# Performance work log

Hardware: AMD Instinct MI355X
Metric: run time of the kernel (lower is better)

The kernel has to match this reference:

```python
import jax, jax.numpy as jnp
import numpy as np

B, S, C = 4096, 512, 8
P, D, H, DFF, NL = 16, 64, 4, 96, 3
HID, HOR = 128, 24
TAU_MIN, TAU_MAX, NSTEPS = 0.05, 5.0, 32


def setup_inputs() -> dict:
    key = jax.random.key(0)
    ks = iter(jax.random.split(key, 40))
    n = lambda shape, s=0.05: (s * jax.random.normal(next(ks), shape)).astype(jnp.float32)
    return {
        "x": jax.random.normal(next(ks), (B, S, C), dtype=jnp.float32),
        "conv_w": n((D, C, P)),
        "conv_b": n((D,)),
        "cls": jax.random.normal(next(ks), (1, 1, D), dtype=jnp.float32),
        "attn_w": n((NL, 3 * D, D)),
        "attn_b": n((NL, 3 * D)),
        "out_w": n((NL, D, D)),
        "out_b": n((NL, D)),
        "ln1_g": jnp.ones((NL, D), jnp.float32),
        "ln1_b": jnp.zeros((NL, D), jnp.float32),
        "ln2_g": jnp.ones((NL, D), jnp.float32),
        "ln2_b": jnp.zeros((NL, D), jnp.float32),
        "ff1_w": n((NL, DFF, D)),
        "ff1_b": n((NL, DFF)),
        "ff2_w": n((NL, D, DFF)),
        "ff2_b": n((NL, D)),
        "B_mat": (0.02 * jax.random.normal(next(ks), (D, D))).astype(jnp.float32),
        "dr1_w": n((HID, D)),
        "dr1_b": n((HID,)),
        "dr2_w": n((D, HID)),
        "dr2_b": n((D,)),
        "tau1_w": n((HID, D + 1)),
        "tau1_b": n((HID,)),
        "tau2_w": n((D, HID)),
        "tau2_b": n((D,)),
        "fc_w": n((HOR * C, D)),
        "fc_b": n((HOR * C,)),
    }


def _layernorm(h, g, b, eps=1e-5):
    m = h.mean(-1, keepdims=True)
    v = ((h - m) ** 2).mean(-1, keepdims=True)
    return (h - m) / jnp.sqrt(v + eps) * g + b


def _pos_enc(L, d, dtype):
    pos = jnp.arange(L, dtype=dtype)[:, None]
    div = jnp.exp(jnp.arange(0, d, 2, dtype=dtype) * (-np.log(10000.0) / d))
    pe = jnp.zeros((L, d), dtype)
    pe = pe.at[:, 0::2].set(jnp.sin(pos * div))
    pe = pe.at[:, 1::2].set(jnp.cos(pos * div))
    return pe


def reference(x, conv_w, conv_b, cls, attn_w, attn_b, out_w, out_b,
              ln1_g, ln1_b, ln2_g, ln2_b, ff1_w, ff1_b, ff2_w, ff2_b,
              B_mat, dr1_w, dr1_b, dr2_w, dr2_b, tau1_w, tau1_b, tau2_w, tau2_b,
              fc_w, fc_b):
    bsz, s, c = x.shape
    n_p = s // P
    # PatchEmbed1D: Conv1d(kernel=stride=P) == per-patch linear projection
    xp = x.reshape(bsz, n_p, P, c)                       # [B,N,P,C]
    z = jnp.einsum('bnpc,dcp->bnd', xp, conv_w) + conv_b  # [B,N,D]
    z = jnp.concatenate([jnp.broadcast_to(cls, (bsz, 1, D)), z], axis=1)  # [B,N+1,D]
    L = z.shape[1]
    z = z + _pos_enc(L, D, z.dtype)
    hd = D // H
    scale = 1.0 / np.sqrt(hd)
    for l in range(NL):
        qkv = z @ attn_w[l].T + attn_b[l]                # [B,L,3D]
        q, k, v = jnp.split(qkv, 3, axis=-1)
        q = q.reshape(bsz, L, H, hd).transpose(0, 2, 1, 3)
        k = k.reshape(bsz, L, H, hd).transpose(0, 2, 1, 3)
        v = v.reshape(bsz, L, H, hd).transpose(0, 2, 1, 3)
        att = jax.nn.softmax(jnp.einsum('bhqd,bhkd->bhqk', q, k) * scale, axis=-1)
        o = jnp.einsum('bhqk,bhkd->bhqd', att, v).transpose(0, 2, 1, 3).reshape(bsz, L, D)
        o = o @ out_w[l].T + out_b[l]
        z = _layernorm(z + o, ln1_g[l], ln1_b[l])        # post-norm (torch default)
        f = jax.nn.relu(z @ ff1_w[l].T + ff1_b[l]) @ ff2_w[l].T + ff2_b[l]
        z = _layernorm(z + f, ln2_g[l], ln2_b[l])
    zc = z[:, 0]                                         # CLS token [B,D]
    # stable linear term A = -B^T B
    A = -(B_mat.T @ B_mat)
    h = 1.0 / NSTEPS

    def step(carry, _):
        zt, t = carry
        drive = jnp.tanh(zt @ dr1_w.T + dr1_b) @ dr2_w.T + dr2_b
        tt = jnp.full((zt.shape[0], 1), t, zt.dtype)
        tau_raw = jnp.tanh(jnp.concatenate([zt, tt], -1) @ tau1_w.T + tau1_b) @ tau2_w.T + tau2_b
        tau = TAU_MIN + (TAU_MAX - TAU_MIN) * jax.nn.sigmoid(jax.nn.softplus(tau_raw) + 1e-6)
        inv = 1.0 / tau
        dz = zt @ A.T + (-inv * zt + inv * drive)
        return (zt + h * dz, t + h), None

    (zt, _), _ = jax.lax.scan(step, (zc, jnp.float32(0.0)), None, length=NSTEPS)
    return zt @ fc_w.T + fc_b                            # [B, horizon*input_dim]
```

## Files before the change

### kernel.cpp

```cpp
#include <hip/hip_runtime.h>
#include <hip/hip_fp16.h>
#include <math.h>

#define DEV static __device__ __forceinline__

typedef _Float16 f16;
typedef __attribute__((ext_vector_type(4))) _Float16 f16x4;
typedef __attribute__((ext_vector_type(8))) _Float16 f16x8;
typedef __attribute__((ext_vector_type(4))) float f32x4;

DEV f16x8 ld8(const f16* p) { return *(const f16x8*)p; }
DEV f32x4 mfma32(f16x8 a, f16x8 b, f32x4 c) {
  return __builtin_amdgcn_mfma_f32_16x16x32_f16(a, b, c, 0, 0, 0);
}
DEV float ftanh(float x) {
  float e = __expf(2.f * x);
  return 1.f - 2.f / (e + 1.f);
}

__global__ __launch_bounds__(64) void prep_kernel(
    const float* __restrict__ Bm,
    const float* __restrict__ dr1_w, const float* __restrict__ dr1_b,
    const float* __restrict__ dr2_w, const float* __restrict__ dr2_b,
    const float* __restrict__ tau1_w, const float* __restrict__ tau1_b,
    const float* __restrict__ tau2_w, const float* __restrict__ tau2_b,
    const float* __restrict__ fc_w, const float* __restrict__ fc_b,
    char* __restrict__ wsb) {
  f16* dr1h = (f16*)(wsb);
  f16* tau1h = (f16*)(wsb + 16384);
  f16* dr2h = (f16*)(wsb + 32768);
  f16* tau2h = (f16*)(wsb + 49152);
  f16* Ah = (f16*)(wsb + 65536);
  f16* fch = (f16*)(wsb + 73728);
  float* fb = (float*)(wsb + 98304);

  const int t = threadIdx.x, blk = blockIdx.x;
  if (blk < 16) {
    int row = blk * 4 + (t >> 4), c0 = 4 * (t & 15);
    float a0 = 0.f, a1 = 0.f, a2 = 0.f, a3 = 0.f;
    for (int m = 0; m < 64; ++m) {
      float br = Bm[m * 64 + row];
      a0 = fmaf(br, Bm[m * 64 + c0 + 0], a0);
      a1 = fmaf(br, Bm[m * 64 + c0 + 1], a1);
      a2 = fmaf(br, Bm[m * 64 + c0 + 2], a2);
      a3 = fmaf(br, Bm[m * 64 + c0 + 3], a3);
    }
    Ah[row * 64 + c0 + 0] = (f16)(-a0);
    Ah[row * 64 + c0 + 1] = (f16)(-a1);
    Ah[row * 64 + c0 + 2] = (f16)(-a2);
    Ah[row * 64 + c0 + 3] = (f16)(-a3);
  } else if (blk < 48) {
    int idx = (blk - 16) * 64 + t;
    int row = idx >> 4, c0 = 4 * (idx & 15);
#pragma unroll
    for (int j = 0; j < 4; ++j) {
      dr1h[row * 64 + c0 + j] = (f16)dr1_w[row * 64 + c0 + j];
      tau1h[row * 64 + c0 + j] = (f16)tau1_w[row * 65 + c0 + j];
    }
  } else if (blk < 80) {
    int idx = (blk - 48) * 64 + t;
    int row = idx >> 5, c0 = 4 * (idx & 31);
#pragma unroll
    for (int j = 0; j < 4; ++j) {
      dr2h[row * 128 + c0 + j] = (f16)dr2_w[row * 128 + c0 + j];
      tau2h[row * 128 + c0 + j] = (f16)tau2_w[row * 128 + c0 + j];
    }
  } else if (blk < 128) {
    int idx = (blk - 80) * 64 + t;
    int row = idx >> 4, c0 = 4 * (idx & 15);
#pragma unroll
    for (int j = 0; j < 4; ++j)
      fch[row * 64 + c0 + j] = (f16)fc_w[row * 64 + c0 + j];
  } else {
    for (int i = (blk - 128) * 64 + t; i < 704; i += 128) {
      float v;
      if (i < 128) v = dr1_b[i];
      else if (i < 256) v = tau1_b[i - 128];
      else if (i < 320) v = dr2_b[i - 256];
      else if (i < 384) v = tau2_b[i - 320];
      else if (i < 512) v = tau1_w[(i - 384) * 65 + 64];
      else v = fc_b[i - 512];
      fb[i] = v;
    }
  }
}

__global__ __launch_bounds__(256) void prep_tf(
    const float* __restrict__ conv_w, const float* __restrict__ attn_w,
    const float* __restrict__ out_w, const float* __restrict__ ff1_w,
    const float* __restrict__ ff2_w, const float* __restrict__ conv_b,
    f16* __restrict__ tfw, float* __restrict__ pecb) {
  int idx = blockIdx.x * 256 + threadIdx.x;
  if (idx >= 96256) return;
  if (idx >= 94208) {
    int e = idx - 94208;
    int i = 1 + (e >> 6), dd = e & 63;
    float freq = __expf(-0.14391157f * (float)(dd & ~1));
    float ang = (float)i * freq;
    pecb[e] = ((dd & 1) ? cosf(ang) : sinf(ang)) + conv_b[dd];
    return;
  }
  float v;
  if (idx < 8192) {
    int dd = idx >> 7, k = idx & 127;
    v = conv_w[dd * 128 + (k & 7) * 16 + (k >> 3)];
  } else {
    int r = idx - 8192;
    int l = r / 28672, q = r - l * 28672;
    if (q < 12288) v = attn_w[l * 12288 + q];
    else if (q < 16384) v = out_w[l * 4096 + (q - 12288)];
    else if (q < 22528) v = ff1_w[l * 6144 + (q - 16384)];
    else v = ff2_w[l * 6144 + (q - 22528)];
  }
  tfw[idx] = (f16)v;
}

__global__ __launch_bounds__(256, 3) void tf_kernel(
    const float* __restrict__ x, const f16* __restrict__ tfw,
    const float* __restrict__ pecb, const float* __restrict__ cls,
    const float* __restrict__ attn_b, const float* __restrict__ out_b,
    const float* __restrict__ ln1_g, const float* __restrict__ ln1_b,
    const float* __restrict__ ln2_g, const float* __restrict__ ln2_b,
    const float* __restrict__ ff1_b, const float* __restrict__ ff2_b,
    float* __restrict__ zc) {
  __shared__ __align__(16) unsigned char SH[52240];
  float* Zm = (float*)SH;
  f16* Zh = (f16*)(SH + 8976);
  f16* Qh = (f16*)(SH + 15888);
  f16* Kh = (f16*)(SH + 22800);
  f16* VT = (f16*)(SH + 29712);
  f16* P = (f16*)(SH + 36880);
  f16* Sx = (f16*)(SH + 15888);
  f16* f1h = (f16*)(SH + 22800);
  f16* oh = Qh;

  const int t = threadIdx.x;
  const int b = blockIdx.x;
  const int w = t >> 6, lane = t & 63;
  const int c16 = lane & 15, q4 = lane >> 4;
  const int dcol = w * 16 + c16;
  const int d4 = w * 16 + q4 * 4;
  const int nrow = t >> 2, nl4 = t & 3;

  {
    const float4* xg = (const float4*)(x + (size_t)b * 4096);
    for (int i = t; i < 1024; i += 256) {
      int n = i >> 5, jj = i & 31;
      float4 v = xg[i];
      *(f16x4*)(Sx + n * 136 + jj * 4) = f16x4{(f16)v.x, (f16)v.y, (f16)v.z, (f16)v.w};
    }
    unsigned* zp = (unsigned*)(Zh + 33 * 72);
    for (int i = t; i < 540; i += 256) zp[i] = 0u;
    uint4 z4{0, 0, 0, 0};
    uint4* pp = (uint4*)P;
    for (int i = t; i < 960; i += 256) pp[i] = z4;
    if (t < 64) {
      float v = cls[t] + ((t & 1) ? 1.0f : 0.0f);
      Zm[t] = v; Zh[t] = (f16)v;
    }
  }
  __syncthreads();

  {
    f16x8 cw[4];
#pragma unroll
    for (int kb = 0; kb < 4; ++kb)
      cw[kb] = ld8(tfw + dcol * 128 + kb * 32 + q4 * 8);
#pragma unroll
    for (int it = 0; it < 2; ++it) {
      f32x4 acc = {};
#pragma unroll
      for (int kb = 0; kb < 4; ++kb)
        acc = mfma32(cw[kb], ld8(Sx + (it * 16 + c16) * 136 + kb * 32 + q4 * 8), acc);
      int n = it * 16 + c16;
      float4 pe = *(const float4*)(pecb + n * 64 + d4);
      float4 o{acc[0] + pe.x, acc[1] + pe.y, acc[2] + pe.z, acc[3] + pe.w};
      *(float4*)(Zm + (n + 1) * 68 + d4) = o;
      *(f16x4*)(Zh + (n + 1) * 72 + d4) = f16x4{(f16)o.x, (f16)o.y, (f16)o.z, (f16)o.w};
    }
  }
  __syncthreads();

  for (int l = 0; l < 3; ++l) {
    const f16* lw = tfw + 8192 + l * 28672;
    const int ntile = (l == 2) ? 1 : 3;
    const bool has2 = (w < 2);
    const int j1f = has2 ? (w + 4) * 16 + c16 : dcol;
    const int j1b = has2 ? (w + 4) * 16 + q4 * 4 : d4;

    f16x8 wq0 = ld8(lw + dcol * 64 + q4 * 8);
    f16x8 wq1 = ld8(lw + dcol * 64 + 32 + q4 * 8);
    f16x8 wk0 = ld8(lw + (64 + dcol) * 64 + q4 * 8);
    f16x8 wk1 = ld8(lw + (64 + dcol) * 64 + 32 + q4 * 8);
    f16x8 wv0 = ld8(lw + (128 + dcol) * 64 + q4 * 8);
    f16x8 wv1 = ld8(lw + (128 + dcol) * 64 + 32 + q4 * 8);
    f16x8 ow0 = ld8(lw + 12288 + dcol * 64 + q4 * 8);
    f16x8 ow1 = ld8(lw + 12288 + dcol * 64 + 32 + q4 * 8);
    f16x8 f1w00 = ld8(lw + 16384 + dcol * 64 + q4 * 8);
    f16x8 f1w01 = ld8(lw + 16384 + dcol * 64 + 32 + q4 * 8);
    f16x8 f1w10 = ld8(lw + 16384 + j1f * 64 + q4 * 8);
    f16x8 f1w11 = ld8(lw + 16384 + j1f * 64 + 32 + q4 * 8);
    f16x8 fw20 = ld8(lw + 22528 + dcol * 96 + q4 * 8);
    f16x8 fw21 = ld8(lw + 22528 + dcol * 96 + 32 + q4 * 8);
    f16x8 fw22 = ld8(lw + 22528 + dcol * 96 + 64 + q4 * 8);
    float4 bq4 = *(const float4*)(attn_b + l * 192 + d4);
    float4 bk4 = *(const float4*)(attn_b + l * 192 + 64 + d4);
    float bv = attn_b[l * 192 + 128 + dcol];
    float4 ob4 = *(const float4*)(out_b + l * 64 + d4);
    float4 f1b0 = *(const float4*)(ff1_b + l * 96 + d4);
    float4 f1b1 = *(const float4*)(ff1_b + l * 96 + j1b);
    float4 f2b4 = *(const float4*)(ff2_b + l * 64 + d4);

    {
      f16x8 zr0[3], zr1[3];
#pragma unroll
      for (int it = 0; it < 3; ++it) {
        zr0[it] = ld8(Zh + (it * 16 + c16) * 72 + q4 * 8);
        zr1[it] = ld8(Zh + (it * 16 + c16) * 72 + 32 + q4 * 8);
      }
#pragma unroll
      for (int it = 0; it < 3; ++it) {
        f32x4 aq = {}, ak = {}, av = {};
        aq = mfma32(wq0, zr0[it], aq); aq = mfma32(wq1, zr1[it], aq);
        ak = mfma32(wk0, zr0[it], ak); ak = mfma32(wk1, zr1[it], ak);
        av = mfma32(zr0[it], wv0, av); av = mfma32(zr1[it], wv1, av);
        int i = it * 16 + c16;
        *(f16x4*)(Qh + i * 72 + d4) =
            f16x4{(f16)((aq[0] + bq4.x) * 0.25f), (f16)((aq[1] + bq4.y) * 0.25f),
                  (f16)((aq[2] + bq4.z) * 0.25f), (f16)((aq[3] + bq4.w) * 0.25f)};
        *(f16x4*)(Kh + i * 72 + d4) =
            f16x4{(f16)(ak[0] + bk4.x), (f16)(ak[1] + bk4.y),
                  (f16)(ak[2] + bk4.z), (f16)(ak[3] + bk4.w)};
        if (it < 2) {
          *(f16x4*)(VT + dcol * 56 + it * 16 + q4 * 4) =
              f16x4{(f16)(av[0] + bv), (f16)(av[1] + bv),
                    (f16)(av[2] + bv), (f16)(av[3] + bv)};
        } else if (q4 == 0) {
          VT[dcol * 56 + 32] = (f16)(av[0] + bv);
        }
      }
    }

    {
      f16x8 zf = {};
      f16x8 kf0 = (q4 < 2) ? ld8(Kh + (c16) * 72 + w * 16 + q4 * 8) : zf;
      f16x8 kf1 = (q4 < 2) ? ld8(Kh + (16 + c16) * 72 + w * 16 + q4 * 8) : zf;
      f16x8 kf2 = (q4 < 2) ? ld8(Kh + (32 + c16) * 72 + w * 16 + q4 * 8) : zf;
      f16x8 vf = ld8(VT + dcol * 56 + q4 * 8);
      float vt32[4];
#pragma unroll
      for (int r = 0; r < 4; ++r) vt32[r] = (float)VT[(d4 + r) * 56 + 32];
      f16* Ph = P + w * 1920;
#pragma unroll
      for (int it = 0; it < 3; ++it) {
        if (it >= ntile) break;
        f16x8 qf = (q4 < 2) ? ld8(Qh + (it * 16 + c16) * 72 + w * 16 + q4 * 8) : zf;
        f32x4 zz = {};
        f32x4 s0 = mfma32(kf0, qf, zz);
        f32x4 s1 = mfma32(kf1, qf, zz);
        f32x4 s2 = mfma32(kf2, qf, zz);
        float m = -1e30f;
#pragma unroll
        for (int r = 0; r < 4; ++r) m = fmaxf(m, fmaxf(s0[r], s1[r]));
        if (q4 == 0) m = fmaxf(m, s2[0]);
        m = fmaxf(m, __shfl_xor(m, 16));
        m = fmaxf(m, __shfl_xor(m, 32));
        float e0[4], e1[4], su = 0.f;
#pragma unroll
        for (int r = 0; r < 4; ++r) {
          e0[r] = __expf(s0[r] - m); e1[r] = __expf(s1[r] - m);
          su += e0[r] + e1[r];
        }
        float e2 = (q4 == 0) ? __expf(s2[0] - m) : 0.f;
        su += e2;
        su += __shfl_xor(su, 16);
        su += __shfl_xor(su, 32);
        float inv = 1.f / su;
        int i = it * 16 + c16;
        *(f16x4*)(Ph + i * 40 + q4 * 4) =
            f16x4{(f16)(e0[0] * inv), (f16)(e0[1] * inv),
                  (f16)(e0[2] * inv), (f16)(e0[3] * inv)};
        *(f16x4*)(Ph + i * 40 + 16 + q4 * 4) =
            f16x4{(f16)(e1[0] * inv), (f16)(e1[1] * inv),
                  (f16)(e1[2] * inv), (f16)(e1[3] * inv)};
        if (q4 == 0) Ph[i * 40 + 32] = (f16)(e2 * inv);
      }
#pragma unroll
      for (int it = 0; it < 3; ++it) {
        if (it >= ntile) break;
        int i = it * 16 + c16;
        f16x8 pf = ld8(Ph + i * 40 + q4 * 8);
        f32x4 zz = {};
        f32x4 acc = mfma32(vf, pf, zz);
        float p32 = (float)Ph[i * 40 + 32];
        *(f16x4*)(oh + i * 72 + d4) =
            f16x4{(f16)(acc[0] + vt32[0] * p32), (f16)(acc[1] + vt32[1] * p32),
                  (f16)(acc[2] + vt32[2] * p32), (f16)(acc[3] + vt32[3] * p32)};
      }
    }
    __syncthreads();

#pragma unroll
    for (int it = 0; it < 3; ++it) {
      if (it >= ntile) break;
      int i = it * 16 + c16;
      f32x4 acc = {};
      acc = mfma32(ow0, ld8(oh + i * 72 + q4 * 8), acc);
      acc = mfma32(ow1, ld8(oh + i * 72 + 32 + q4 * 8), acc);
      if (it < 2 || c16 == 0) {
        float4 z = *(float4*)(Zm + i * 68 + d4);
        z.x += acc[0] + ob4.x; z.y += acc[1] + ob4.y;
        z.z += acc[2] + ob4.z; z.w += acc[3] + ob4.w;
        *(float4*)(Zm + i * 68 + d4) = z;
      }
    }
    __syncthreads();

    {
      int rows = (l == 2) ? 16 : 33;
      if (nrow < rows) {
        const float4* zr = (const float4*)(Zm + nrow * 68 + nl4 * 16);
        float4 zv[4];
        float su = 0.f, ss = 0.f;
#pragma unroll
        for (int g4 = 0; g4 < 4; ++g4) {
          float4 v = zr[g4];
          zv[g4] = v;
          su += (v.x + v.y) + (v.z + v.w);
          ss = fmaf(v.x, v.x, ss); ss = fmaf(v.y, v.y, ss);
          ss = fmaf(v.z, v.z, ss); ss = fmaf(v.w, v.w, ss);
        }
        su += __shfl_xor(su, 1); ss += __shfl_xor(ss, 1);
        su += __shfl_xor(su, 2); ss += __shfl_xor(ss, 2);
        float m = su * 0.015625f;
        float rr = rsqrtf(ss * 0.015625f - m * m + 1e-5f);
        const float4* gg = (const float4*)(ln1_g + l * 64 + nl4 * 16);
        const float4* bb = (const float4*)(ln1_b + l * 64 + nl4 * 16);
        float4* zw = (float4*)(Zm + nrow * 68 + nl4 * 16);
        f16* zh = Zh + nrow * 72 + nl4 * 16;
#pragma unroll
        for (int g4 = 0; g4 < 4; ++g4) {
          float4 G = gg[g4], B = bb[g4], v = zv[g4];
          float4 o;
          o.x = (v.x - m) * rr * G.x + B.x;
          o.y = (v.y - m) * rr * G.y + B.y;
          o.z = (v.z - m) * rr * G.z + B.z;
          o.w = (v.w - m) * rr * G.w + B.w;
          zw[g4] = o;
          *(f16x4*)(zh + g4 * 4) = f16x4{(f16)o.x, (f16)o.y, (f16)o.z, (f16)o.w};
        }
      }
    }
    __syncthreads();

    {
      f16x8 zr0[3], zr1[3];
#pragma unroll
      for (int it = 0; it < 3; ++it) {
        zr0[it] = ld8(Zh + (it * 16 + c16) * 72 + q4 * 8);
        zr1[it] = ld8(Zh + (it * 16 + c16) * 72 + 32 + q4 * 8);
      }
#pragma unroll
      for (int it = 0; it < 3; ++it) {
        if (it >= ntile) break;
        int i = it * 16 + c16;
        f32x4 acc = {};
        acc = mfma32(f1w00, zr0[it], acc);
        acc = mfma32(f1w01, zr1[it], acc);
        *(f16x4*)(f1h + i * 104 + d4) =
            f16x4{(f16)fmaxf(acc[0] + f1b0.x, 0.f), (f16)fmaxf(acc[1] + f1b0.y, 0.f),
                  (f16)fmaxf(acc[2] + f1b0.z, 0.f), (f16)fmaxf(acc[3] + f1b0.w, 0.f)};
        if (has2) {
          f32x4 a2 = {};
          a2 = mfma32(f1w10, zr0[it], a2);
          a2 = mfma32(f1w11, zr1[it], a2);
          *(f16x4*)(f1h + i * 104 + j1b) =
              f16x4{(f16)fmaxf(a2[0] + f1b1.x, 0.f), (f16)fmaxf(a2[1] + f1b1.y, 0.f),
                    (f16)fmaxf(a2[2] + f1b1.z, 0.f), (f16)fmaxf(a2[3] + f1b1.w, 0.f)};
        }
      }
    }
    __syncthreads();

#pragma unroll
    for (int it = 0; it < 3; ++it) {
      if (it >= ntile) break;
      int i = it * 16 + c16;
      f32x4 acc = {};
      acc = mfma32(fw20, ld8(f1h + i * 104 + q4 * 8), acc);
      acc = mfma32(fw21, ld8(f1h + i * 104 + 32 + q4 * 8), acc);
      acc = mfma32(fw22, ld8(f1h + i * 104 + 64 + q4 * 8), acc);
      if (it < 2 || c16 == 0) {
        float4 z = *(float4*)(Zm + i * 68 + d4);
        z.x += acc[0] + f2b4.x; z.y += acc[1] + f2b4.y;
        z.z += acc[2] + f2b4.z; z.w += acc[3] + f2b4.w;
        *(float4*)(Zm + i * 68 + d4) = z;
      }
    }
    __syncthreads();

    {
      int rows = (l == 2) ? 1 : 33;
      if (nrow < rows) {
        const float4* zr = (const float4*)(Zm + nrow * 68 + nl4 * 16);
        float4 zv[4];
        float su = 0.f, ss = 0.f;
#pragma unroll
        for (int g4 = 0; g4 < 4; ++g4) {
          float4 v = zr[g4];
          zv[g4] = v;
          su += (v.x + v.y) + (v.z + v.w);
          ss = fmaf(v.x, v.x, ss); ss = fmaf(v.y, v.y, ss);
          ss = fmaf(v.z, v.z, ss); ss = fmaf(v.w, v.w, ss);
        }
        su += __shfl_xor(su, 1); ss += __shfl_xor(ss, 1);
        su += __shfl_xor(su, 2); ss += __shfl_xor(ss, 2);
        float m = su * 0.015625f;
        float rr = rsqrtf(ss * 0.015625f - m * m + 1e-5f);
        const float4* gg = (const float4*)(ln2_g + l * 64 + nl4 * 16);
        const float4* bb = (const float4*)(ln2_b + l * 64 + nl4 * 16);
        if (l == 2) {
          float4* zo = (float4*)(zc + (size_t)b * 64 + nl4 * 16);
#pragma unroll
          for (int g4 = 0; g4 < 4; ++g4) {
            float4 G = gg[g4], B = bb[g4], v = zv[g4];
            float4 o;
            o.x = (v.x - m) * rr * G.x + B.x;
            o.y = (v.y - m) * rr * G.y + B.y;
            o.z = (v.z - m) * rr * G.z + B.z;
            o.w = (v.w - m) * rr * G.w + B.w;
            zo[g4] = o;
          }
        } else {
          float4* zw = (float4*)(Zm + nrow * 68 + nl4 * 16);
          f16* zh = Zh + nrow * 72 + nl4 * 16;
#pragma unroll
          for (int g4 = 0; g4 < 4; ++g4) {
            float4 G = gg[g4], B = bb[g4], v = zv[g4];
            float4 o;
            o.x = (v.x - m) * rr * G.x + B.x;
            o.y = (v.y - m) * rr * G.y + B.y;
            o.z = (v.z - m) * rr * G.z + B.z;
            o.w = (v.w - m) * rr * G.w + B.w;
            zw[g4] = o;
            *(f16x4*)(zh + g4 * 4) = f16x4{(f16)o.x, (f16)o.y, (f16)o.z, (f16)o.w};
          }
        }
      }
    }
    __syncthreads();
  }
}

__global__ __launch_bounds__(256, 1) void ode_kernel(
    const char* __restrict__ wsb, const float* __restrict__ zc,
    float* __restrict__ out) {
  const f16* dr1h = (const f16*)(wsb);
  const f16* tau1h = (const f16*)(wsb + 16384);
  const f16* Ah = (const f16*)(wsb + 65536);
  const f16* fch = (const f16*)(wsb + 73728);
  const float* fb = (const float*)(wsb + 98304);

  __shared__ __align__(16) f16 dr2s[64 * 128];
  __shared__ __align__(16) f16 tau2s[64 * 128];
  __shared__ __align__(16) f16 ztL[16 * 64];
  __shared__ __align__(16) f16 hdL[16 * 128];
  __shared__ __align__(16) f16 htL[16 * 128];

  const int t = threadIdx.x;
  const int w = t >> 6;
  const int lane = t & 63;
  const int c16 = lane & 15, q4 = lane >> 4;
  const int b0 = blockIdx.x * 16;
  const int swz = (c16 & 7) << 3;

  for (int i = t; i < 2048; i += 256) {
    int m = i >> 10, gi = i & 1023, row = gi >> 4, g = gi & 15;
    uint4 v = ((const uint4*)(wsb + 32768 + m * 16384))[gi];
    ((uint4*)(m ? tau2s : dr2s))[row * 16 + (g ^ (row & 7))] = v;
  }

  f16x8 dr1B[2][2], tau1B[2][2], AB[2];
#pragma unroll
  for (int j = 0; j < 2; ++j) {
    int cth = w * 2 + j;
#pragma unroll
    for (int kb = 0; kb < 2; ++kb) {
      dr1B[j][kb] = ld8(dr1h + (cth * 16 + c16) * 64 + kb * 32 + q4 * 8);
      tau1B[j][kb] = ld8(tau1h + (cth * 16 + c16) * 64 + kb * 32 + q4 * 8);
    }
  }
#pragma unroll
  for (int kb = 0; kb < 2; ++kb)
    AB[kb] = ld8(Ah + (w * 16 + c16) * 64 + kb * 32 + q4 * 8);
  float dr1b[2], tau1b[2], t1t[2];
#pragma unroll
  for (int j = 0; j < 2; ++j) {
    int cc = (w * 2 + j) * 16 + c16;
    dr1b[j] = fb[cc]; tau1b[j] = fb[128 + cc]; t1t[j] = fb[384 + cc];
  }
  float dr2b = fb[256 + w * 16 + c16];
  float tau2b = fb[320 + w * 16 + c16];

  float zt[4];
#pragma unroll
  for (int r = 0; r < 4; ++r)
    zt[r] = zc[(size_t)(b0 + q4 * 4 + r) * 64 + w * 16 + c16];

  __syncthreads();

  float tm = 0.f;
  for (int s = 0; s < 32; ++s) {
#pragma unroll
    for (int r = 0; r < 4; ++r) {
      int row = q4 * 4 + r;
      ztL[row * 64 + ((w * 16 + c16) ^ ((row & 7) << 3))] = (f16)zt[r];
    }
    __syncthreads();
    f16x8 ztA[2];
#pragma unroll
    for (int kb = 0; kb < 2; ++kb)
      ztA[kb] = ld8(ztL + c16 * 64 + ((kb * 32 + q4 * 8) ^ swz));

#pragma unroll
    for (int j = 0; j < 2; ++j) {
      f32x4 ad = {}, at = {};
      ad = mfma32(ztA[0], dr1B[j][0], ad);
      ad = mfma32(ztA[1], dr1B[j][1], ad);
      at = mfma32(ztA[0], tau1B[j][0], at);
      at = mfma32(ztA[1], tau1B[j][1], at);
      float bt = fmaf(tm, t1t[j], tau1b[j]);
      int colbase = (w * 2 + j) * 16 + c16;
#pragma unroll
      for (int r = 0; r < 4; ++r) {
        int row = q4 * 4 + r;
        int off = row * 128 + (colbase ^ ((row & 7) << 3));
        hdL[off] = (f16)ftanh(ad[r] + dr1b[j]);
        htL[off] = (f16)ftanh(at[r] + bt);
      }
    }
    __syncthreads();
    f16x8 hdA[4], htA[4];
#pragma unroll
    for (int kb = 0; kb < 4; ++kb) {
      int ko = c16 * 128 + ((kb * 32 + q4 * 8) ^ swz);
      hdA[kb] = ld8(hdL + ko);
      htA[kb] = ld8(htL + ko);
    }

    {
      int row16 = (w * 16 + c16) * 128;
      f32x4 dv = {}, tr = {}, za = {};
#pragma unroll
      for (int kb = 0; kb < 4; ++kb) {
        f16x8 bd = ld8(dr2s + row16 + ((kb * 32 + q4 * 8) ^ swz));
        f16x8 bt2 = ld8(tau2s + row16 + ((kb * 32 + q4 * 8) ^ swz));
        dv = mfma32(hdA[kb], bd, dv);
        tr = mfma32(htA[kb], bt2, tr);
      }
      za = mfma32(ztA[0], AB[0], za);
      za = mfma32(ztA[1], AB[1], za);
#pragma unroll
      for (int r = 0; r < 4; ++r) {
        float traw = tr[r] + tau2b;
        float sp = (traw > 15.f) ? traw : log1pf(__expf(traw));
        float sg = 1.f / (1.f + __expf(-(sp + 1e-6f)));
        float inv = 1.f / fmaf(4.95f, sg, 0.05f);
        float ztv = zt[r];
        float dz = za[r] + inv * ((dv[r] + dr2b) - ztv);
        zt[r] = fmaf(0.03125f, dz, ztv);
      }
    }
    tm += 0.03125f;
  }

#pragma unroll
  for (int r = 0; r < 4; ++r) {
    int row = q4 * 4 + r;
    ztL[row * 64 + ((w * 16 + c16) ^ ((row & 7) << 3))] = (f16)zt[r];
  }
  __syncthreads();
  f16x8 zA2[2];
#pragma unroll
  for (int kb = 0; kb < 2; ++kb)
    zA2[kb] = ld8(ztL + c16 * 64 + ((kb * 32 + q4 * 8) ^ swz));
#pragma unroll
  for (int j = 0; j < 3; ++j) {
    int ct = w * 3 + j;
    f32x4 acc = {};
    acc = mfma32(zA2[0], ld8(fch + (ct * 16 + c16) * 64 + q4 * 8), acc);
    acc = mfma32(zA2[1], ld8(fch + (ct * 16 + c16) * 64 + 32 + q4 * 8), acc);
    float bias = fb[512 + ct * 16 + c16];
#pragma unroll
    for (int r = 0; r < 4; ++r)
      out[(size_t)(b0 + q4 * 4 + r) * 192 + ct * 16 + c16] = acc[r] + bias;
  }
}

extern "C" void kernel_launch(void* const* d_in, const int* in_sizes, int n_in,
                              void* d_out, int out_size, void* d_ws, size_t ws_size,
                              hipStream_t stream) {
  const float* x = (const float*)d_in[0];
  const float* conv_w = (const float*)d_in[1];
  const float* conv_b = (const float*)d_in[2];
  const float* cls = (const float*)d_in[3];
  const float* attn_w = (const float*)d_in[4];
  const float* attn_b = (const float*)d_in[5];
  const float* out_w = (const float*)d_in[6];
  const float* out_b = (const float*)d_in[7];
  const float* ln1_g = (const float*)d_in[8];
  const float* ln1_b = (const float*)d_in[9];
  const float* ln2_g = (const float*)d_in[10];
  const float* ln2_b = (const float*)d_in[11];
  const float* ff1_w = (const float*)d_in[12];
  const float* ff1_b = (const float*)d_in[13];
  const float* ff2_w = (const float*)d_in[14];
  const float* ff2_b = (const float*)d_in[15];
  const float* B_mat = (const float*)d_in[16];
  const float* dr1_w = (const float*)d_in[17];
  const float* dr1_b = (const float*)d_in[18];
  const float* dr2_w = (const float*)d_in[19];
  const float* dr2_b = (const float*)d_in[20];
  const float* tau1_w = (const float*)d_in[21];
  const float* tau1_b = (const float*)d_in[22];
  const float* tau2_w = (const float*)d_in[23];
  const float* tau2_b = (const float*)d_in[24];
  const float* fc_w = (const float*)d_in[25];
  const float* fc_b = (const float*)d_in[26];

  char* wsb = (char*)d_ws;
  float* zcb = (float*)(wsb + 101376);
  f16* tfw = (f16*)(wsb + 1149952);
  float* pecb = (float*)(wsb + 1338368);

  prep_kernel<<<130, 64, 0, stream>>>(B_mat, dr1_w, dr1_b, dr2_w, dr2_b,
                                      tau1_w, tau1_b, tau2_w, tau2_b,
                                      fc_w, fc_b, wsb);
  prep_tf<<<376, 256, 0, stream>>>(conv_w, attn_w, out_w, ff1_w, ff2_w, conv_b,
                                   tfw, pecb);
  tf_kernel<<<4096, 256, 0, stream>>>(x, tfw, pecb, cls, attn_b, out_b,
                                      ln1_g, ln1_b, ln2_g, ln2_b, ff1_b, ff2_b, zcb);
  ode_kernel<<<256, 256, 0, stream>>>(wsb, zcb, (float*)d_out);
}
```

Baseline: 269.7 us.

## Drop fp32 residual buffer in transformer LDS and split ODE batch across more blocks

The transformer kernel drops its fp32 residual copy and keeps the residual stream only in fp16 shared memory. The VT and P buffers are compacted, which cuts LDS from about 52KB to 39KB so four blocks can fit per CU instead of three. The ODE kernel now handles 8 batch rows per block over 512 blocks, with the 16-row MFMA tile half duplicated, so more of the GPU is used on the serial 32-step loop. The cost is fp16 rounding on the residual accumulation, and half of the ODE MFMA work is redundant.

```diff
diff --git a/kernel.cpp b/kernel.cpp
--- a/kernel.cpp
+++ b/kernel.cpp
@@ -115,7 +115,7 @@
   tfw[idx] = (f16)v;
 }
 
-__global__ __launch_bounds__(256, 3) void tf_kernel(
+__global__ __launch_bounds__(256, 4) void tf_kernel(
     const float* __restrict__ x, const f16* __restrict__ tfw,
     const float* __restrict__ pecb, const float* __restrict__ cls,
     const float* __restrict__ attn_b, const float* __restrict__ out_b,
@@ -123,15 +123,14 @@
     const float* __restrict__ ln2_g, const float* __restrict__ ln2_b,
     const float* __restrict__ ff1_b, const float* __restrict__ ff2_b,
     float* __restrict__ zc) {
-  __shared__ __align__(16) unsigned char SH[52240];
-  float* Zm = (float*)SH;
-  f16* Zh = (f16*)(SH + 8976);
-  f16* Qh = (f16*)(SH + 15888);
-  f16* Kh = (f16*)(SH + 22800);
-  f16* VT = (f16*)(SH + 29712);
-  f16* P = (f16*)(SH + 36880);
-  f16* Sx = (f16*)(SH + 15888);
-  f16* f1h = (f16*)(SH + 22800);
+  __shared__ __align__(16) unsigned char SH[38800];
+  f16* Zh = (f16*)SH;
+  f16* Qh = (f16*)(SH + 6912);
+  f16* Kh = (f16*)(SH + 13824);
+  f16* VT = (f16*)(SH + 20736);
+  f16* P = (f16*)(SH + 25856);
+  f16* Sx = (f16*)(SH + 6912);
+  f16* f1h = (f16*)(SH + 13824);
   f16* oh = Qh;
 
   const int t = threadIdx.x;
@@ -153,11 +152,8 @@
     for (int i = t; i < 540; i += 256) zp[i] = 0u;
     uint4 z4{0, 0, 0, 0};
     uint4* pp = (uint4*)P;
-    for (int i = t; i < 960; i += 256) pp[i] = z4;
-    if (t < 64) {
-      float v = cls[t] + ((t & 1) ? 1.0f : 0.0f);
-      Zm[t] = v; Zh[t] = (f16)v;
-    }
+    for (int i = t; i < 809; i += 256) pp[i] = z4;
+    if (t < 64) Zh[t] = (f16)(cls[t] + ((t & 1) ? 1.0f : 0.0f));
   }
   __syncthreads();
 
@@ -174,9 +170,9 @@
         acc = mfma32(cw[kb], ld8(Sx + (it * 16 + c16) * 136 + kb * 32 + q4 * 8), acc);
       int n = it * 16 + c16;
       float4 pe = *(const float4*)(pecb + n * 64 + d4);
-      float4 o{acc[0] + pe.x, acc[1] + pe.y, acc[2] + pe.z, acc[3] + pe.w};
-      *(float4*)(Zm + (n + 1) * 68 + d4) = o;
-      *(f16x4*)(Zh + (n + 1) * 72 + d4) = f16x4{(f16)o.x, (f16)o.y, (f16)o.z, (f16)o.w};
+      *(f16x4*)(Zh + (n + 1) * 72 + d4) =
+          f16x4{(f16)(acc[0] + pe.x), (f16)(acc[1] + pe.y),
+                (f16)(acc[2] + pe.z), (f16)(acc[3] + pe.w)};
     }
   }
   __syncthreads();
@@ -232,11 +228,11 @@
             f16x4{(f16)(ak[0] + bk4.x), (f16)(ak[1] + bk4.y),
                   (f16)(ak[2] + bk4.z), (f16)(ak[3] + bk4.w)};
         if (it < 2) {
-          *(f16x4*)(VT + dcol * 56 + it * 16 + q4 * 4) =
+          *(f16x4*)(VT + dcol * 40 + it * 16 + q4 * 4) =
               f16x4{(f16)(av[0] + bv), (f16)(av[1] + bv),
                     (f16)(av[2] + bv), (f16)(av[3] + bv)};
         } else if (q4 == 0) {
-          VT[dcol * 56 + 32] = (f16)(av[0] + bv);
+          VT[dcol * 40 + 32] = (f16)(av[0] + bv);
         }
       }
     }
@@ -246,11 +242,11 @@
       f16x8 kf0 = (q4 < 2) ? ld8(Kh + (c16) * 72 + w * 16 + q4 * 8) : zf;
       f16x8 kf1 = (q4 < 2) ? ld8(Kh + (16 + c16) * 72 + w * 16 + q4 * 8) : zf;
       f16x8 kf2 = (q4 < 2) ? ld8(Kh + (32 + c16) * 72 + w * 16 + q4 * 8) : zf;
-      f16x8 vf = ld8(VT + dcol * 56 + q4 * 8);
+      f16x8 vf = ld8(VT + dcol * 40 + q4 * 8);
       float vt32[4];
 #pragma unroll
-      for (int r = 0; r < 4; ++r) vt32[r] = (float)VT[(d4 + r) * 56 + 32];
-      f16* Ph = P + w * 1920;
+      for (int r = 0; r < 4; ++r) vt32[r] = (float)VT[(d4 + r) * 40 + 32];
+      f16* Ph = P + w * 1320;
 #pragma unroll
       for (int it = 0; it < 3; ++it) {
         if (it >= ntile) break;
@@ -277,13 +273,15 @@
         su += __shfl_xor(su, 32);
         float inv = 1.f / su;
         int i = it * 16 + c16;
-        *(f16x4*)(Ph + i * 40 + q4 * 4) =
-            f16x4{(f16)(e0[0] * inv), (f16)(e0[1] * inv),
-                  (f16)(e0[2] * inv), (f16)(e0[3] * inv)};
-        *(f16x4*)(Ph + i * 40 + 16 + q4 * 4) =
-            f16x4{(f16)(e1[0] * inv), (f16)(e1[1] * inv),
-                  (f16)(e1[2] * inv), (f16)(e1[3] * inv)};
-        if (q4 == 0) Ph[i * 40 + 32] = (f16)(e2 * inv);
+        if (i < 33) {
+          *(f16x4*)(Ph + i * 40 + q4 * 4) =
+              f16x4{(f16)(e0[0] * inv), (f16)(e0[1] * inv),
+                    (f16)(e0[2] * inv), (f16)(e0[3] * inv)};
+          *(f16x4*)(Ph + i * 40 + 16 + q4 * 4) =
+              f16x4{(f16)(e1[0] * inv), (f16)(e1[1] * inv),
+                    (f16)(e1[2] * inv), (f16)(e1[3] * inv)};
+          if (q4 == 0) Ph[i * 40 + 32] = (f16)(e2 * inv);
+        }
       }
 #pragma unroll
       for (int it = 0; it < 3; ++it) {
@@ -308,10 +306,12 @@
       acc = mfma32(ow0, ld8(oh + i * 72 + q4 * 8), acc);
       acc = mfma32(ow1, ld8(oh + i * 72 + 32 + q4 * 8), acc);
       if (it < 2 || c16 == 0) {
-        float4 z = *(float4*)(Zm + i * 68 + d4);
-        z.x += acc[0] + ob4.x; z.y += acc[1] + ob4.y;
-        z.z += acc[2] + ob4.z; z.w += acc[3] + ob4.w;
-        *(float4*)(Zm + i * 68 + d4) = z;
+        f16x4 zr = *(f16x4*)(Zh + i * 72 + d4);
+        *(f16x4*)(Zh + i * 72 + d4) =
+            f16x4{(f16)((float)zr[0] + acc[0] + ob4.x),
+                  (f16)((float)zr[1] + acc[1] + ob4.y),
+                  (f16)((float)zr[2] + acc[2] + ob4.z),
+                  (f16)((float)zr[3] + acc[3] + ob4.w)};
       }
     }
     __syncthreads();
@@ -319,35 +319,28 @@
     {
       int rows = (l == 2) ? 16 : 33;
       if (nrow < rows) {
-        const float4* zr = (const float4*)(Zm + nrow * 68 + nl4 * 16);
-        float4 zv[4];
+        f16* zr = Zh + nrow * 72 + nl4 * 16;
+        f16x8 h0 = ld8(zr), h1 = ld8(zr + 8);
+        float v[16];
+#pragma unroll
+        for (int j = 0; j < 8; ++j) { v[j] = (float)h0[j]; v[8 + j] = (float)h1[j]; }
         float su = 0.f, ss = 0.f;
 #pragma unroll
-        for (int g4 = 0; g4 < 4; ++g4) {
-          float4 v = zr[g4];
-          zv[g4] = v;
-          su += (v.x + v.y) + (v.z + v.w);
-          ss = fmaf(v.x, v.x, ss); ss = fmaf(v.y, v.y, ss);
-          ss = fmaf(v.z, v.z, ss); ss = fmaf(v.w, v.w, ss);
-        }
+        for (int j = 0; j < 16; ++j) { su += v[j]; ss = fmaf(v[j], v[j], ss); }
         su += __shfl_xor(su, 1); ss += __shfl_xor(ss, 1);
         su += __shfl_xor(su, 2); ss += __shfl_xor(ss, 2);
         float m = su * 0.015625f;
         float rr = rsqrtf(ss * 0.015625f - m * m + 1e-5f);
         const float4* gg = (const float4*)(ln1_g + l * 64 + nl4 * 16);
         const float4* bb = (const float4*)(ln1_b + l * 64 + nl4 * 16);
-        float4* zw = (float4*)(Zm + nrow * 68 + nl4 * 16);
-        f16* zh = Zh + nrow * 72 + nl4 * 16;
 #pragma unroll
         for (int g4 = 0; g4 < 4; ++g4) {
-          float4 G = gg[g4], B = bb[g4], v = zv[g4];
-          float4 o;
-          o.x = (v.x - m) * rr * G.x + B.x;
-          o.y = (v.y - m) * rr * G.y + B.y;
-          o.z = (v.z - m) * rr * G.z + B.z;
-          o.w = (v.w - m) * rr * G.w + B.w;
-          zw[g4] = o;
-          *(f16x4*)(zh + g4 * 4) = f16x4{(f16)o.x, (f16)o.y, (f16)o.z, (f16)o.w};
+          float4 G = gg[g4], B = bb[g4];
+          *(f16x4*)(zr + g4 * 4) =
+              f16x4{(f16)((v[g4 * 4 + 0] - m) * rr * G.x + B.x),
+                    (f16)((v[g4 * 4 + 1] - m) * rr * G.y + B.y),
+                    (f16)((v[g4 * 4 + 2] - m) * rr * G.z + B.z),
+                    (f16)((v[g4 * 4 + 3] - m) * rr * G.w + B.w)};
         }
       }
     }
@@ -391,10 +384,12 @@
       acc = mfma32(fw21, ld8(f1h + i * 104 + 32 + q4 * 8), acc);
       acc = mfma32(fw22, ld8(f1h + i * 104 + 64 + q4 * 8), acc);
       if (it < 2 || c16 == 0) {
-        float4 z = *(float4*)(Zm + i * 68 + d4);
-        z.x += acc[0] + f2b4.x; z.y += acc[1] + f2b4.y;
-        z.z += acc[2] + f2b4.z; z.w += acc[3] + f2b4.w;
-        *(float4*)(Zm + i * 68 + d4) = z;
+        f16x4 zr = *(f16x4*)(Zh + i * 72 + d4);
+        *(f16x4*)(Zh + i * 72 + d4) =
+            f16x4{(f16)((float)zr[0] + acc[0] + f2b4.x),
+                  (f16)((float)zr[1] + acc[1] + f2b4.y),
+                  (f16)((float)zr[2] + acc[2] + f2b4.z),
+                  (f16)((float)zr[3] + acc[3] + f2b4.w)};
       }
     }
     __syncthreads();
@@ -402,17 +397,14 @@
     {
       int rows = (l == 2) ? 1 : 33;
       if (nrow < rows) {
-        const float4* zr = (const float4*)(Zm + nrow * 68 + nl4 * 16);
-        float4 zv[4];
+        f16* zr = Zh + nrow * 72 + nl4 * 16;
+        f16x8 h0 = ld8(zr), h1 = ld8(zr + 8);
+        float v[16];
+#pragma unroll
+        for (int j = 0; j < 8; ++j) { v[j] = (float)h0[j]; v[8 + j] = (float)h1[j]; }
         float su = 0.f, ss = 0.f;
 #pragma unroll
-        for (int g4 = 0; g4 < 4; ++g4) {
-          float4 v = zr[g4];
-          zv[g4] = v;
-          su += (v.x + v.y) + (v.z + v.w);
-          ss = fmaf(v.x, v.x, ss); ss = fmaf(v.y, v.y, ss);
-          ss = fmaf(v.z, v.z, ss); ss = fmaf(v.w, v.w, ss);
-        }
+        for (int j = 0; j < 16; ++j) { su += v[j]; ss = fmaf(v[j], v[j], ss); }
         su += __shfl_xor(su, 1); ss += __shfl_xor(ss, 1);
         su += __shfl_xor(su, 2); ss += __shfl_xor(ss, 2);
         float m = su * 0.015625f;
@@ -423,27 +415,21 @@
           float4* zo = (float4*)(zc + (size_t)b * 64 + nl4 * 16);
 #pragma unroll
           for (int g4 = 0; g4 < 4; ++g4) {
-            float4 G = gg[g4], B = bb[g4], v = zv[g4];
-            float4 o;
-            o.x = (v.x - m) * rr * G.x + B.x;
-            o.y = (v.y - m) * rr * G.y + B.y;
-            o.z = (v.z - m) * rr * G.z + B.z;
-            o.w = (v.w - m) * rr * G.w + B.w;
-            zo[g4] = o;
+            float4 G = gg[g4], B = bb[g4];
+            zo[g4] = make_float4((v[g4 * 4 + 0] - m) * rr * G.x + B.x,
+                                 (v[g4 * 4 + 1] - m) * rr * G.y + B.y,
+                                 (v[g4 * 4 + 2] - m) * rr * G.z + B.z,
+                                 (v[g4 * 4 + 3] - m) * rr * G.w + B.w);
           }
         } else {
-          float4* zw = (float4*)(Zm + nrow * 68 + nl4 * 16);
-          f16* zh = Zh + nrow * 72 + nl4 * 16;
 #pragma unroll
           for (int g4 = 0; g4 < 4; ++g4) {
-            float4 G = gg[g4], B = bb[g4], v = zv[g4];
-            float4 o;
-            o.x = (v.x - m) * rr * G.x + B.x;
-            o.y = (v.y - m) * rr * G.y + B.y;
-            o.z = (v.z - m) * rr * G.z + B.z;
-            o.w = (v.w - m) * rr * G.w + B.w;
-            zw[g4] = o;
-            *(f16x4*)(zh + g4 * 4) = f16x4{(f16)o.x, (f16)o.y, (f16)o.z, (f16)o.w};
+            float4 G = gg[g4], B = bb[g4];
+            *(f16x4*)(zr + g4 * 4) =
+                f16x4{(f16)((v[g4 * 4 + 0] - m) * rr * G.x + B.x),
+                      (f16)((v[g4 * 4 + 1] - m) * rr * G.y + B.y),
+                      (f16)((v[g4 * 4 + 2] - m) * rr * G.z + B.z),
+                      (f16)((v[g4 * 4 + 3] - m) * rr * G.w + B.w)};
           }
         }
       }
@@ -452,7 +438,7 @@
   }
 }
 
-__global__ __launch_bounds__(256, 1) void ode_kernel(
+__global__ __launch_bounds__(256, 2) void ode_kernel(
     const char* __restrict__ wsb, const float* __restrict__ zc,
     float* __restrict__ out) {
   const f16* dr1h = (const f16*)(wsb);
@@ -471,7 +457,7 @@
   const int w = t >> 6;
   const int lane = t & 63;
   const int c16 = lane & 15, q4 = lane >> 4;
-  const int b0 = blockIdx.x * 16;
+  const int b0 = blockIdx.x * 8;
   const int swz = (c16 & 7) << 3;
 
   for (int i = t; i < 2048; i += 256) {
@@ -504,8 +490,10 @@
 
   float zt[4];
 #pragma unroll
-  for (int r = 0; r < 4; ++r)
-    zt[r] = zc[(size_t)(b0 + q4 * 4 + r) * 64 + w * 16 + c16];
+  for (int r = 0; r < 4; ++r) {
+    int gr = (q4 * 4 + r) & 7;
+    zt[r] = zc[(size_t)(b0 + gr) * 64 + w * 16 + c16];
+  }
 
   __syncthreads();
 
@@ -591,9 +579,11 @@
     acc = mfma32(zA2[0], ld8(fch + (ct * 16 + c16) * 64 + q4 * 8), acc);
     acc = mfma32(zA2[1], ld8(fch + (ct * 16 + c16) * 64 + 32 + q4 * 8), acc);
     float bias = fb[512 + ct * 16 + c16];
-#pragma unroll
-    for (int r = 0; r < 4; ++r)
-      out[(size_t)(b0 + q4 * 4 + r) * 192 + ct * 16 + c16] = acc[r] + bias;
+    if (q4 < 2) {
+#pragma unroll
+      for (int r = 0; r < 4; ++r)
+        out[(size_t)(b0 + q4 * 4 + r) * 192 + ct * 16 + c16] = acc[r] + bias;
+    }
   }
 }
 
@@ -640,5 +630,5 @@
                                    tfw, pecb);
   tf_kernel<<<4096, 256, 0, stream>>>(x, tfw, pecb, cls, attn_b, out_b,
                                       ln1_g, ln1_b, ln2_g, ln2_b, ff1_b, ff2_b, zcb);
-  ode_kernel<<<256, 256, 0, stream>>>(wsb, zcb, (float*)d_out);
+  ode_kernel<<<512, 256, 0, stream>>>(wsb, zcb, (float*)d_out);
 }
```

New measurement: 351.0 us. 30.1% more time.
